# Optimization experiments

Hardware: AMD Instinct MI355X
Metric: run time of the kernel (lower is better)

The kernel has to match this reference:

```python
import jax, jax.numpy as jnp
import numpy as np

NUM_TAGS = 256
BATCH = 64
SEQ = 1024


def setup_inputs() -> dict:
    key = jax.random.key(0)
    k1, k2, k3, k4, k5 = jax.random.split(key, 5)
    emissions = jax.random.normal(k1, (BATCH, SEQ, NUM_TAGS), dtype=jnp.float32)
    tags = jax.random.randint(k2, (BATCH, SEQ), 0, NUM_TAGS, dtype=jnp.int64)
    mask = jnp.ones((BATCH, SEQ), dtype=bool)
    # params mimic nn.init.uniform_(-0.1, 0.1)
    transitions = jax.random.uniform(k3, (NUM_TAGS, NUM_TAGS), jnp.float32, -0.1, 0.1)
    start_transitions = jax.random.uniform(k4, (NUM_TAGS,), jnp.float32, -0.1, 0.1)
    end_transitions = jax.random.uniform(k5, (NUM_TAGS,), jnp.float32, -0.1, 0.1)
    return {
        "emissions": emissions,
        "transitions": transitions,
        "start_transitions": start_transitions,
        "end_transitions": end_transitions,
        "tags": tags,
        "mask": mask,
    }


def _compute_normalizer(emissions, mask, transitions, start_transitions, end_transitions):
    # emissions: [B,S,T], mask: [B,S] bool
    score0 = start_transitions[None, :] + emissions[:, 0]  # [B,T]

    def step(score, xs):
        em_i, m_i = xs  # em_i: [B,T], m_i: [B]
        # [B, prev, next]
        next_score = jax.nn.logsumexp(
            score[:, :, None] + transitions[None, :, :] + em_i[:, None, :], axis=1
        )
        score = jnp.where(m_i[:, None], next_score, score)
        return score, None

    em_rest = jnp.swapaxes(emissions[:, 1:], 0, 1)  # [S-1,B,T]
    mk_rest = jnp.swapaxes(mask[:, 1:], 0, 1)       # [S-1,B]
    score, _ = jax.lax.scan(step, score0, (em_rest, mk_rest))
    return jax.nn.logsumexp(score + end_transitions[None, :], axis=1)  # [B]


def _compute_score(emissions, tags, mask, transitions, start_transitions, end_transitions):
    # gather emission score of the gold tag at each position: [B,S]
    em_g = jnp.take_along_axis(emissions, tags[:, :, None], axis=2)[:, :, 0]
    # transitions indexed [cur_tag, prev_tag] to match the torch code exactly
    trans_g = transitions[tags[:, 1:], tags[:, :-1]]  # [B,S-1]
    mf = mask[:, 1:].astype(emissions.dtype)
    score = start_transitions[tags[:, 0]] + em_g[:, 0]
    score = score + jnp.sum((trans_g + em_g[:, 1:]) * mf, axis=1)
    seq_ends = mask.astype(jnp.int32).sum(axis=1) - 1  # [B]
    last_tags = jnp.take_along_axis(tags, seq_ends[:, None].astype(tags.dtype), axis=1)[:, 0]
    return score + end_transitions[last_tags]


def reference(emissions, transitions, start_transitions, end_transitions, tags, mask):
    nll = _compute_normalizer(emissions, mask, transitions, start_transitions, end_transitions) \
        - _compute_score(emissions, tags, mask, transitions, start_transitions, end_transitions)
    return jnp.mean(nll)  # reduction='mean'
```

## Files before the change

kernel.cpp:

```cpp
#include <hip/hip_runtime.h>
#include <math.h>

#define NTAGS 256
#define BATCH 64
#define SEQ   1024
#define BPB   16
#define NBLK  (BATCH / BPB)

typedef float f32x4 __attribute__((ext_vector_type(4)));
typedef short bf16x8 __attribute__((ext_vector_type(8)));

__device__ __forceinline__ unsigned short rne_bf16(float x) {
    unsigned u = __float_as_uint(x);
    return (unsigned short)((u + 0x7FFFu + ((u >> 16) & 1u)) >> 16);
}
__device__ __forceinline__ unsigned cvt_pk_bf16(float lo, float hi) {
    unsigned r;
    asm("v_cvt_pk_bf16_f32 %0, %1, %2" : "=v"(r) : "v"(lo), "v"(hi));
    return r;
}
__device__ __forceinline__ void lds_barrier() {
    asm volatile("s_waitcnt lgkmcnt(0)\n\ts_barrier" ::: "memory");
}

__global__ __launch_bounds__(512)
void crf_normalizer_kernel(
    const float* __restrict__ em,
    const float* __restrict__ trans,
    const float* __restrict__ startT,
    const float* __restrict__ endT,
    float* __restrict__ norm_out)
{
    const int tid = threadIdx.x;
    const int w   = tid >> 6;
    const int l   = tid & 63;
    const int l15 = l & 15;
    const int hi  = (l >> 4) & 3;
    const int bb0 = blockIdx.x * BPB;

    __shared__ __align__(16) unsigned short Vb[2][BPB * NTAGS];
    __shared__ __align__(16) float Rld[2][BPB];
    __shared__ __align__(16) float P2[BPB][BPB];

    bf16x8 Af[2][8];
#pragma unroll
    for (int mt = 0; mt < 2; ++mt) {
        const int j = ((w << 1) + mt) * 16 + l15;
#pragma unroll
        for (int kk = 0; kk < 8; ++kk) {
            bf16x8 v;
#pragma unroll
            for (int e = 0; e < 8; ++e)
                v[e] = (short)rne_bf16(__expf(trans[(kk * 32 + hi * 8 + e) * NTAGS + j]));
            Af[mt][kk] = v;
        }
    }

    if (tid < 256) {
        const int b  = tid & 15;
        const int jg = tid >> 4;
        const float* e0 = em + (size_t)(bb0 + b) * SEQ * NTAGS + jg * 16;
        float vals[16];
#pragma unroll
        for (int q = 0; q < 4; ++q) {
            f32x4 ev = *reinterpret_cast<const f32x4*>(&e0[q * 4]);
            f32x4 sv = *reinterpret_cast<const f32x4*>(&startT[jg * 16 + q * 4]);
#pragma unroll
            for (int c = 0; c < 4; ++c)
                vals[q * 4 + c] = __expf(ev[c] + sv[c]);
        }
#pragma unroll
        for (int half = 0; half < 2; ++half) {
            unsigned pk[4];
#pragma unroll
            for (int q = 0; q < 4; ++q)
                pk[q] = cvt_pk_bf16(vals[half * 8 + 2 * q], vals[half * 8 + 2 * q + 1]);
            const int byte = b * 512 + ((jg * 32 + half * 16) ^ ((b & 7) << 4));
            *reinterpret_cast<uint4*>(reinterpret_cast<char*>(&Vb[0][0]) + byte) =
                *reinterpret_cast<const uint4*>(pk);
        }
        if (jg == 0)
            Rld[0][b] = __expf(-(startT[0] + em[(size_t)(bb0 + b) * SEQ * NTAGS]));
    }

    int boffh[8];
#pragma unroll
    for (int kk = 0; kk < 8; ++kk)
        boffh[kk] = (l15 * 512 + ((kk * 64 + hi * 16) ^ ((l15 & 7) << 4))) >> 1;
    int woff[2];
#pragma unroll
    for (int mt = 0; mt < 2; ++mt) {
        const int gmt = (w << 1) + mt;
        woff[mt] = l15 * 512 + ((gmt * 32 + hi * 8) ^ ((l15 & 7) << 4));
    }

    const float* emP = em + ((size_t)(bb0 + l15) * SEQ + 1) * NTAGS + (w << 5) + (hi << 2);
    f32x4 emA0 = *reinterpret_cast<const f32x4*>(emP);
    f32x4 emA1 = *reinterpret_cast<const f32x4*>(emP + 16);
    f32x4 emB0 = *reinterpret_cast<const f32x4*>(emP + NTAGS);
    f32x4 emB1 = *reinterpret_cast<const f32x4*>(emP + NTAGS + 16);

    double S = 0.0;
    __syncthreads();

#define CRF_STEP(PR, EM0, EM1, DOPREF)                                        \
    do {                                                                      \
        const float q_ = Rld[(PR)][l15];                \
        bf16x8 Bf0[4];                                                        \
        _Pragma("unroll")                                                     \
        for (int kk = 0; kk < 4; ++kk)                                        \
            Bf0[kk] = *reinterpret_cast<const bf16x8*>(&Vb[(PR)][boffh[kk]]); \
        f32x4 xf0, xf1;                                                       \
        xf0[0] = __expf(EM0[0]); xf0[1] = __expf(EM0[1]);                     \
        xf0[2] = __expf(EM0[2]); xf0[3] = __expf(EM0[3]);                     \
        xf1[0] = __expf(EM1[0]); xf1[1] = __expf(EM1[1]);                     \
        xf1[2] = __expf(EM1[2]); xf1[3] = __expf(EM1[3]);                     \
        if (DOPREF) {     \
            EM0 = *reinterpret_cast<const f32x4*>(emP + 2 * NTAGS);           \
            EM1 = *reinterpret_cast<const f32x4*>(emP + 2 * NTAGS + 16);      \
        }                                                                     \
        emP += NTAGS;                                                         \
        f32x4 ac0 = {0,0,0,0}, ac1 = {0,0,0,0};                               \
        _Pragma("unroll")                                                     \
        for (int kk = 0; kk < 4; ++kk) {                                      \
            ac0 = __builtin_amdgcn_mfma_f32_16x16x32_bf16(Af[0][kk], Bf0[kk], ac0, 0, 0, 0); \
            ac1 = __builtin_amdgcn_mfma_f32_16x16x32_bf16(Af[1][kk], Bf0[kk], ac1, 0, 0, 0); \
        }                                                                     \
        bf16x8 Bf1[4];                                                        \
        _Pragma("unroll")                                                     \
        for (int kk = 0; kk < 4; ++kk)                                        \
            Bf1[kk] = *reinterpret_cast<const bf16x8*>(&Vb[(PR)][boffh[kk + 4]]); \
        _Pragma("unroll")                                                     \
        for (int kk = 0; kk < 4; ++kk) {                                      \
            ac0 = __builtin_amdgcn_mfma_f32_16x16x32_bf16(Af[0][kk + 4], Bf1[kk], ac0, 0, 0, 0); \
            ac1 = __builtin_amdgcn_mfma_f32_16x16x32_bf16(Af[1][kk + 4], Bf1[kk], ac1, 0, 0, 0); \
        }                                                                     \
        const f32x4 cf0 = xf0 * q_;                                           \
        const f32x4 cf1 = xf1 * q_;                                           \
        const f32x4 sv0 = ac0 * cf0;                                          \
        const f32x4 sv1 = ac1 * cf1;                                          \
        char* const wbase = reinterpret_cast<char*>(&Vb[1 - (PR)][0]);        \
        uint2 p0, p1;                                                         \
        p0.x = cvt_pk_bf16(sv0[0], sv0[1]); p0.y = cvt_pk_bf16(sv0[2], sv0[3]); \
        p1.x = cvt_pk_bf16(sv1[0], sv1[1]); p1.y = cvt_pk_bf16(sv1[2], sv1[3]); \
        *reinterpret_cast<uint2*>(wbase + woff[0]) = p0;                      \
        *reinterpret_cast<uint2*>(wbase + woff[1]) = p1;                      \
        if (tid < 16) {                                                       \
            S -= (double)__logf(q_);                                          \
            Rld[1 - (PR)][l15] = __builtin_amdgcn_rcpf(ac0[0] * cf0[0]);      \
        }                                                                     \
        lds_barrier();                                                        \
    } while (0)

    for (int u = 0; u < 510; ++u) {
        CRF_STEP(0, emA0, emA1, 1);
        CRF_STEP(1, emB0, emB1, 1);
    }
    CRF_STEP(0, emA0, emA1, 1);
    CRF_STEP(1, emB0, emB1, 0);
    CRF_STEP(0, emA0, emA1, 0);
#undef CRF_STEP

    __syncthreads();

    if (tid < 256) {
        const int b  = tid & 15;
        const int jg = tid >> 4;
        float accv = 0.f;
#pragma unroll
        for (int half = 0; half < 2; ++half) {
            const int byte = b * 512 + ((jg * 32 + half * 16) ^ ((b & 7) << 4));
            bf16x8 vv = *reinterpret_cast<const bf16x8*>(
                reinterpret_cast<const char*>(&Vb[1][0]) + byte);
#pragma unroll
            for (int e = 0; e < 8; ++e) {
                const float f = __uint_as_float(((unsigned)(unsigned short)vv[e]) << 16);
                accv += f * __expf(endT[jg * 16 + half * 8 + e]);
            }
        }
        P2[b][jg] = accv;
    }
    __syncthreads();
    if (tid < 16) {
        float tot = 0.f;
#pragma unroll
        for (int g = 0; g < 16; ++g) tot += P2[tid][g];
        norm_out[bb0 + tid] = (float)(S + (double)__logf(tot));
    }
}

__global__ __launch_bounds__(256) void crf_score_kernel(
    const float* __restrict__ em,
    const float* __restrict__ trans,
    const float* __restrict__ startT,
    const float* __restrict__ endT,
    const int* __restrict__ tags,
    float* __restrict__ score_out)
{
    const int b   = blockIdx.x;
    const int tid = threadIdx.x;
    const int* tg = tags + b * SEQ;
    const float* emb = em + (size_t)b * SEQ * NTAGS;

    float s = 0.f;
    for (int t = tid; t < SEQ; t += 256) {
        int cur = tg[t];
        float v = emb[t * NTAGS + cur];
        v += (t == 0) ? startT[cur] : trans[cur * NTAGS + tg[t - 1]];
        s += v;
    }
    __shared__ float red[4];
#pragma unroll
    for (int off = 32; off > 0; off >>= 1)
        s += __shfl_xor(s, off);
    if ((tid & 63) == 0) red[tid >> 6] = s;
    __syncthreads();
    if (tid == 0)
        score_out[b] = red[0] + red[1] + red[2] + red[3] + endT[tg[SEQ - 1]];
}

__global__ void crf_finalize_kernel(const float* __restrict__ norm,
                                    const float* __restrict__ score,
                                    float* __restrict__ out)
{
    const int tid = threadIdx.x;
    float v = norm[tid] - score[tid];
#pragma unroll
    for (int off = 32; off > 0; off >>= 1)
        v += __shfl_xor(v, off);
    if (tid == 0) out[0] = v * (1.0f / BATCH);
}

extern "C" void kernel_launch(void* const* d_in, const int* in_sizes, int n_in,
                              void* d_out, int out_size, void* d_ws, size_t ws_size,
                              hipStream_t stream)
{
    const float* em     = (const float*)d_in[0];
    const float* trans  = (const float*)d_in[1];
    const float* startT = (const float*)d_in[2];
    const float* endT   = (const float*)d_in[3];
    const int*   tags   = (const int*)d_in[4];

    float* ws    = (float*)d_ws;
    float* norm  = ws;
    float* score = ws + BATCH;

    crf_normalizer_kernel<<<NBLK, 512, 0, stream>>>(em, trans, startT, endT, norm);
    crf_score_kernel<<<BATCH, 256, 0, stream>>>(em, trans, startT, endT, tags, score);
    crf_finalize_kernel<<<1, 64, 0, stream>>>(norm, score, (float*)d_out);
}
```

Baseline: 473.5 us.

## Pack two batch groups into one 1024-thread normalizer block

The normalizer kernel now runs two independent 16-sequence groups inside one 1024-thread workgroup, with separate LDS buffers per group. The launch goes from four 512-thread blocks to two 1024-thread blocks. The aim is to interleave the two latency-bound recurrences on one CU so each hides the other's stalls. In exchange, both groups share every per-step barrier and compete for the same CU's SIMDs and MFMA units. The 1024-thread launch bound also tightens the per-thread register budget, which may cause spills given the large persistent A fragments.

Result: slower. 919.4 us (+94.2%).

```diff
diff --git a/kernel.cpp b/kernel.cpp
--- a/kernel.cpp
+++ b/kernel.cpp
@@ -5,7 +5,8 @@
 #define BATCH 64
 #define SEQ   1024
 #define BPB   16
-#define NBLK  (BATCH / BPB)
+#define GPB   2
+#define NBLK  (BATCH / (BPB * GPB))
 
 typedef float f32x4 __attribute__((ext_vector_type(4)));
 typedef short bf16x8 __attribute__((ext_vector_type(8)));
@@ -23,7 +24,7 @@
     asm volatile("s_waitcnt lgkmcnt(0)\n\ts_barrier" ::: "memory");
 }
 
-__global__ __launch_bounds__(512)
+__global__ __launch_bounds__(1024)
 void crf_normalizer_kernel(
     const float* __restrict__ em,
     const float* __restrict__ trans,
@@ -31,16 +32,21 @@
     const float* __restrict__ endT,
     float* __restrict__ norm_out)
 {
-    const int tid = threadIdx.x;
-    const int w   = tid >> 6;
-    const int l   = tid & 63;
-    const int l15 = l & 15;
-    const int hi  = (l >> 4) & 3;
-    const int bb0 = blockIdx.x * BPB;
-
-    __shared__ __align__(16) unsigned short Vb[2][BPB * NTAGS];
-    __shared__ __align__(16) float Rld[2][BPB];
-    __shared__ __align__(16) float P2[BPB][BPB];
+    const int tid  = threadIdx.x;
+    const int grp  = tid >> 9;
+    const int ttid = tid & 511;
+    const int w    = ttid >> 6;
+    const int l    = tid & 63;
+    const int l15  = l & 15;
+    const int hi   = (l >> 4) & 3;
+    const int bb0  = blockIdx.x * (BPB * GPB) + grp * BPB;
+
+    __shared__ __align__(16) unsigned short Vb[GPB][2][BPB * NTAGS];
+    __shared__ __align__(16) float Rld[GPB][2][BPB];
+    __shared__ __align__(16) float P2[GPB][BPB][BPB];
+
+    unsigned short* const VbG  = &Vb[grp][0][0];
+    float* const           RldG = &Rld[grp][0][0];
 
     bf16x8 Af[2][8];
 #pragma unroll
@@ -56,9 +62,9 @@
         }
     }
 
-    if (tid < 256) {
-        const int b  = tid & 15;
-        const int jg = tid >> 4;
+    if (ttid < 256) {
+        const int b  = ttid & 15;
+        const int jg = ttid >> 4;
         const float* e0 = em + (size_t)(bb0 + b) * SEQ * NTAGS + jg * 16;
         float vals[16];
 #pragma unroll
@@ -76,11 +82,11 @@
             for (int q = 0; q < 4; ++q)
                 pk[q] = cvt_pk_bf16(vals[half * 8 + 2 * q], vals[half * 8 + 2 * q + 1]);
             const int byte = b * 512 + ((jg * 32 + half * 16) ^ ((b & 7) << 4));
-            *reinterpret_cast<uint4*>(reinterpret_cast<char*>(&Vb[0][0]) + byte) =
+            *reinterpret_cast<uint4*>(reinterpret_cast<char*>(VbG) + byte) =
                 *reinterpret_cast<const uint4*>(pk);
         }
         if (jg == 0)
-            Rld[0][b] = __expf(-(startT[0] + em[(size_t)(bb0 + b) * SEQ * NTAGS]));
+            RldG[b] = __expf(-(startT[0] + em[(size_t)(bb0 + b) * SEQ * NTAGS]));
     }
 
     int boffh[8];
@@ -105,17 +111,18 @@
 
 #define CRF_STEP(PR, EM0, EM1, DOPREF)                                        \
     do {                                                                      \
-        const float q_ = Rld[(PR)][l15];                \
+        const float q_ = RldG[(PR) * BPB + l15];        \
         bf16x8 Bf0[4];                                                        \
         _Pragma("unroll")                                                     \
         for (int kk = 0; kk < 4; ++kk)                                        \
-            Bf0[kk] = *reinterpret_cast<const bf16x8*>(&Vb[(PR)][boffh[kk]]); \
+            Bf0[kk] = *reinterpret_cast<const bf16x8*>(                       \
+                &VbG[(PR) * 4096 + boffh[kk]]);                               \
         f32x4 xf0, xf1;                                                       \
         xf0[0] = __expf(EM0[0]); xf0[1] = __expf(EM0[1]);                     \
         xf0[2] = __expf(EM0[2]); xf0[3] = __expf(EM0[3]);                     \
         xf1[0] = __expf(EM1[0]); xf1[1] = __expf(EM1[1]);                     \
         xf1[2] = __expf(EM1[2]); xf1[3] = __expf(EM1[3]);                     \
-        if (DOPREF) {     \
+        if (DOPREF) {           \
             EM0 = *reinterpret_cast<const f32x4*>(emP + 2 * NTAGS);           \
             EM1 = *reinterpret_cast<const f32x4*>(emP + 2 * NTAGS + 16);      \
         }                                                                     \
@@ -129,7 +136,8 @@
         bf16x8 Bf1[4];                                                        \
         _Pragma("unroll")                                                     \
         for (int kk = 0; kk < 4; ++kk)                                        \
-            Bf1[kk] = *reinterpret_cast<const bf16x8*>(&Vb[(PR)][boffh[kk + 4]]); \
+            Bf1[kk] = *reinterpret_cast<const bf16x8*>(                       \
+                &VbG[(PR) * 4096 + boffh[kk + 4]]);                           \
         _Pragma("unroll")                                                     \
         for (int kk = 0; kk < 4; ++kk) {                                      \
             ac0 = __builtin_amdgcn_mfma_f32_16x16x32_bf16(Af[0][kk + 4], Bf1[kk], ac0, 0, 0, 0); \
@@ -139,15 +147,16 @@
         const f32x4 cf1 = xf1 * q_;                                           \
         const f32x4 sv0 = ac0 * cf0;                                          \
         const f32x4 sv1 = ac1 * cf1;                                          \
-        char* const wbase = reinterpret_cast<char*>(&Vb[1 - (PR)][0]);        \
+        char* const wbase = reinterpret_cast<char*>(VbG) + (1 - (PR)) * 8192; \
         uint2 p0, p1;                                                         \
         p0.x = cvt_pk_bf16(sv0[0], sv0[1]); p0.y = cvt_pk_bf16(sv0[2], sv0[3]); \
         p1.x = cvt_pk_bf16(sv1[0], sv1[1]); p1.y = cvt_pk_bf16(sv1[2], sv1[3]); \
         *reinterpret_cast<uint2*>(wbase + woff[0]) = p0;                      \
         *reinterpret_cast<uint2*>(wbase + woff[1]) = p1;                      \
-        if (tid < 16) {                                                       \
+        if (ttid < 16) {                                                      \
             S -= (double)__logf(q_);                                          \
-            Rld[1 - (PR)][l15] = __builtin_amdgcn_rcpf(ac0[0] * cf0[0]);      \
+            RldG[(1 - (PR)) * BPB + l15] =                                    \
+                __builtin_amdgcn_rcpf(ac0[0] * cf0[0]);       \
         }                                                                     \
         lds_barrier();                                                        \
     } while (0)
@@ -163,29 +172,29 @@
 
     __syncthreads();
 
-    if (tid < 256) {
-        const int b  = tid & 15;
-        const int jg = tid >> 4;
+    if (ttid < 256) {
+        const int b  = ttid & 15;
+        const int jg = ttid >> 4;
         float accv = 0.f;
 #pragma unroll
         for (int half = 0; half < 2; ++half) {
-            const int byte = b * 512 + ((jg * 32 + half * 16) ^ ((b & 7) << 4));
+            const int byte = 8192 + b * 512 + ((jg * 32 + half * 16) ^ ((b & 7) << 4));
             bf16x8 vv = *reinterpret_cast<const bf16x8*>(
-                reinterpret_cast<const char*>(&Vb[1][0]) + byte);
+                reinterpret_cast<const char*>(VbG) + byte);
 #pragma unroll
             for (int e = 0; e < 8; ++e) {
                 const float f = __uint_as_float(((unsigned)(unsigned short)vv[e]) << 16);
                 accv += f * __expf(endT[jg * 16 + half * 8 + e]);
             }
         }
-        P2[b][jg] = accv;
-    }
-    __syncthreads();
-    if (tid < 16) {
+        P2[grp][b][jg] = accv;
+    }
+    __syncthreads();
+    if (ttid < 16) {
         float tot = 0.f;
 #pragma unroll
-        for (int g = 0; g < 16; ++g) tot += P2[tid][g];
-        norm_out[bb0 + tid] = (float)(S + (double)__logf(tot));
+        for (int g = 0; g < 16; ++g) tot += P2[grp][ttid][g];
+        norm_out[bb0 + ttid] = (float)(S + (double)__logf(tot));
     }
 }
 
@@ -245,7 +254,7 @@
     float* norm  = ws;
     float* score = ws + BATCH;
 
-    crf_normalizer_kernel<<<NBLK, 512, 0, stream>>>(em, trans, startT, endT, norm);
+    crf_normalizer_kernel<<<NBLK, 1024, 0, stream>>>(em, trans, startT, endT, norm);
     crf_score_kernel<<<BATCH, 256, 0, stream>>>(em, trans, startT, endT, tags, score);
     crf_finalize_kernel<<<1, 64, 0, stream>>>(norm, score, (float*)d_out);
 }
```
